# Kernel optimization log

Measured on AMD Instinct MI355X. Metric: run time of the kernel, lower is better.

## Reference

```python
import jax, jax.numpy as jnp
import numpy as np

K = 15  # window_size


def setup_inputs() -> dict:
    key = jax.random.key(0)
    k1, k2, k3, k4 = jax.random.split(key, 4)
    x = jax.random.normal(k1, (8, 256, 240, 240), dtype=jnp.float32)
    wq = jax.random.normal(k2, (144, 256), dtype=jnp.float32) * (1.0 / np.sqrt(256))
    wk = jax.random.normal(k3, (144, 256), dtype=jnp.float32) * (1.0 / np.sqrt(256))
    wproj = jax.random.normal(k4, (256, 256), dtype=jnp.float32) * (1.0 / np.sqrt(256))
    return {"x": x, "wq": wq, "wk": wk, "wproj": wproj}


def _pnlm(x, wq, wk, wproj):
    b, c, h, w = x.shape
    ph, pw = (-h) % K, (-w) % K
    if ph or pw:
        x_pad = jnp.pad(x, ((0, 0), (0, 0), (0, ph), (0, pw)), mode='reflect')
    else:
        x_pad = x
    H, W = x_pad.shape[2], x_pad.shape[3]
    nh, nw = H // K, W // K
    N = K * K  # tokens per window
    # blockify: (B,C,H,W) -> (B*nh*nw, C, N)
    blocks = (x_pad.reshape(b, c, nh, K, nw, K)
              .transpose(0, 2, 4, 1, 3, 5)
              .reshape(b * nh * nw, c, N))
    q = jnp.einsum('ec,bcn->bne', wq, blocks)   # (B', N, E)
    km = jnp.einsum('ec,bcm->bem', wk, blocks)  # (B', E, N)
    att = jnp.einsum('bne,bem->bnm', q, km)     # (B', N, N)
    scale = 1.0 / jnp.sqrt(jnp.asarray(q.shape[-1], dtype=att.dtype))
    att = jax.nn.softmax(att * scale, axis=-1)
    y = jnp.einsum('bnm,bcm->bcn', att, blocks)  # att @ V, V = blocks^T
    y = jnp.einsum('oc,bcn->bon', wproj, y)      # 1x1 proj_out
    # unblockify: (B', C, N) -> (B, C, H, W)
    y = (y.reshape(b, nh, nw, c, K, K)
         .transpose(0, 3, 1, 4, 2, 5)
         .reshape(b, c, H, W))
    y = y[:, :, :h, :w]
    return x + y


def reference(x, wq, wk, wproj):
    return _pnlm(x, wq, wk, wproj)
```

## Files before the change

kernel.cpp:

```cpp
#include <hip/hip_runtime.h>


typedef __bf16 bf16x8 __attribute__((ext_vector_type(8)));
typedef float  f32x4  __attribute__((ext_vector_type(4)));

#define MFMA(a,b,c) __builtin_amdgcn_mfma_f32_16x16x32_bf16((a),(b),(c),0,0,0)

#define QK_ROW 320
#define KL_STRIDE 168
#define XBB_ROW 240

__device__ __forceinline__ unsigned short f2bf(float f){
  union { float f; unsigned int u; } v; v.f = f;
  unsigned int r = v.u + 0x7FFFu + ((v.u >> 16) & 1u);
  return (unsigned short)(r >> 16);
}
__device__ __forceinline__ float bf2f(unsigned short u){
  union { unsigned int u; float f; } v; v.u = ((unsigned int)u) << 16;
  return v.f;
}
__device__ __forceinline__ int swz(int row, int col){
  return row*256 + ((((col >> 3) ^ (row & 7)) << 3) | (col & 7));
}
__device__ __forceinline__ int swzC(int row, int col){
  return row*256 + (col ^ ((((row >> 3) ^ row) & 7) << 3));
}
__device__ __forceinline__ bf16x8 ld_frag_lds(const unsigned short* p, int idx){
  uint4 v = *(const uint4*)(p + idx);
  return __builtin_bit_cast(bf16x8, v);
}
__device__ __forceinline__ bf16x8 ld_frag_b(const void* p){
  uint4 v = *(const uint4*)(p);
  return __builtin_bit_cast(bf16x8, v);
}

__device__ __forceinline__ void repack_frag(const unsigned int* plo, const unsigned int* phi,
                                            uint4* outf, int lane){
  const int nn = lane & 15, hh = lane >> 4;
  const int sla = nn + 32*(hh & 1);
  const int slb = sla + 16;
  const bool up = hh >= 2;
  #pragma unroll
  for (int k = 0; k < 8; ++k){
    unsigned int a0 = (unsigned int)__shfl((int)plo[2*k],   sla);
    unsigned int a1 = (unsigned int)__shfl((int)plo[2*k+1], sla);
    unsigned int b0 = (unsigned int)__shfl((int)phi[2*k],   sla);
    unsigned int b1 = (unsigned int)__shfl((int)phi[2*k+1], sla);
    unsigned int c0 = (unsigned int)__shfl((int)plo[2*k],   slb);
    unsigned int c1 = (unsigned int)__shfl((int)plo[2*k+1], slb);
    unsigned int d0 = (unsigned int)__shfl((int)phi[2*k],   slb);
    unsigned int d1 = (unsigned int)__shfl((int)phi[2*k+1], slb);
    outf[k] = make_uint4(up?a1:a0, up?b1:b0, up?c1:c0, up?d1:d0);
  }
}

__global__ __launch_bounds__(256) void k_w(
    const float* __restrict__ wq, const float* __restrict__ wk,
    const float* __restrict__ wproj,
    unsigned short* __restrict__ wqb, unsigned short* __restrict__ wkb,
    unsigned short* __restrict__ wpb)
{
  int i = blockIdx.x*256 + threadIdx.x;
  if (i < 20480){
    int e = i >> 7, c = (i & 127)*2;
    unsigned int v = 0;
    if (e < 144) v = (unsigned int)f2bf(wq[e*256+c]) | ((unsigned int)f2bf(wq[e*256+c+1]) << 16);
    *(unsigned int*)(wqb + (size_t)i*2) = v;
  } else if (i < 40960){
    int j = i - 20480;
    int e = j >> 7, c = (j & 127)*2;
    unsigned int v = 0;
    if (e < 144) v = (unsigned int)f2bf(wk[e*256+c]) | ((unsigned int)f2bf(wk[e*256+c+1]) << 16);
    *(unsigned int*)(wkb + (size_t)j*2) = v;
  } else if (i < 73728){
    int l = i - 40960;
    int o = l >> 7, c = (l & 127)*2;
    *(unsigned int*)(wpb + (size_t)l*2) =
        (unsigned int)f2bf(wproj[o*256+c]) | ((unsigned int)f2bf(wproj[o*256+c+1]) << 16);
  }
}

__global__ __launch_bounds__(256) void k_xb(
    const float* __restrict__ x, unsigned short* __restrict__ xbb)
{
  __shared__ unsigned short xs[8*15*240];
  const int wg = blockIdx.x;
  const int cg = wg & 31;
  const int th = (wg >> 5) & 15;
  const int b  = wg >> 9;
  const int tid = threadIdx.x;

  const float* xb = x + ((size_t)b*256 + cg*8)*57600 + th*15*240;
  for (int i = tid; i < 8*15*120; i += 256){
    int c = i / 1800;
    int rem = i - c*1800;
    int r = rem / 120, p2 = rem - r*120;
    float2 v = *(const float2*)(xb + (size_t)c*57600 + r*240 + p2*2);
    *(unsigned int*)(&xs[(c*15 + r)*240 + p2*2]) =
        (unsigned int)f2bf(v.x) | ((unsigned int)f2bf(v.y) << 16);
  }
  __syncthreads();

  for (int i = tid; i < 8*16*30; i += 256){
    int c = i / 480;
    int rem = i - c*480;
    int tw = rem / 30, ch = rem - tw*30;
    union { unsigned short u16[8]; uint4 u4; } pk;
    #pragma unroll
    for (int j = 0; j < 8; ++j){
      int m = ch*8 + j;
      int r = m / 15, s = m - r*15;
      pk.u16[j] = (m <= 224) ? xs[(c*15 + r)*240 + tw*15 + s] : (unsigned short)0;
    }
    *(uint4*)(xbb + ((size_t)(b*256 + th*16 + tw)*256 + cg*8 + c)*XBB_ROW + ch*8) = pk.u4;
  }
}

__global__ __launch_bounds__(512) void k_qkb(
    const unsigned short* __restrict__ xbb,
    const unsigned short* __restrict__ wqb, const unsigned short* __restrict__ wkb,
    unsigned short* __restrict__ qkws)
{
  __shared__ __align__(16) unsigned short S[32768];
  unsigned short* xt  = S;
  unsigned short* wqs = S;
  unsigned short* wks = S + 8192;
  const int wg = blockIdx.x;
  const int b  = wg >> 8;
  const int th = (wg >> 4) & 15, tw = wg & 15;
  const int h0 = th*15, w0 = tw*15;
  const int tid = threadIdx.x;
  const int lane = tid & 63, wave = tid >> 6;
  const int col  = lane & 15, hi = lane >> 4;
  const unsigned short* xbw = xbb + (size_t)wg * (256*XBB_ROW);

  #pragma unroll 1
  for (int half = 0; half < 2; ++half){
    if (half) __syncthreads();
    for (int i = tid; i < 256*16; i += 512){
      int c = i >> 4, m8 = i & 15;
      int m = half*128 + m8*8;
      if (m < 240){
        uint4 v = *(const uint4*)(xbw + (size_t)c*XBB_ROW + m);
        const unsigned short* pv = (const unsigned short*)&v;
        #pragma unroll
        for (int j = 0; j < 8; ++j)
          xt[swzC(m8*8 + j, c)] = pv[j];
      }
    }
    __syncthreads();

    const int t = half*8 + wave;
    const bool act = t < 15;
    bf16x8 af[8];
    if (act){
      const int rloc = wave*16 + col;
      #pragma unroll
      for (int k = 0; k < 8; ++k)
        af[k] = ld_frag_lds(xt, swzC(rloc, k*32 + hi*8));
    }
    __syncthreads();

    #pragma unroll 1
    for (int eg = 0; eg < 5; ++eg){
      if (eg) __syncthreads();
      for (int i = tid; i < 32*32; i += 512){
        int e_l = i >> 5, c8 = (i & 31)*8;
        size_t off = (size_t)(eg*32 + e_l)*256 + c8;
        *(uint4*)(&wqs[swz(e_l, c8)]) = *(const uint4*)(wqb + off);
        *(uint4*)(&wks[swz(e_l, c8)]) = *(const uint4*)(wkb + off);
      }
      __syncthreads();
      if (act){
        #pragma unroll
        for (int et = 0; et < 2; ++et){
          f32x4 aq = {0.f,0.f,0.f,0.f}, ak = {0.f,0.f,0.f,0.f};
          const int el = et*16 + col;
          #pragma unroll
          for (int k = 0; k < 8; ++k){
            int idx = swz(el, k*32 + hi*8);
            bf16x8 bq = ld_frag_lds(wqs, idx);
            bf16x8 bk = ld_frag_lds(wks, idx);
            aq = MFMA(af[k], bq, aq);
            ak = MFMA(af[k], bk, ak);
          }
          const int e_out = eg*32 + et*16 + col;
          #pragma unroll
          for (int jj = 0; jj < 4; ++jj){
            int m_px = t*16 + hi*4 + jj;
            if (m_px <= 224){
              int hw = (h0 + m_px/15)*240 + w0 + m_px%15;
              size_t row = ((size_t)b*57600 + hw)*QK_ROW;
              qkws[row + e_out]       = f2bf(aq[jj]);
              qkws[row + 160 + e_out] = f2bf(ak[jj]);
            }
          }
        }
      }
    }
  }
}

__global__ __launch_bounds__(512) void k_qk(
    const float* __restrict__ x, const float* __restrict__ wq,
    const float* __restrict__ wk,
    unsigned short* __restrict__ qkws)
{
  __shared__ __align__(16) unsigned short S[32768];
  unsigned short* xt  = S;
  unsigned short* wqs = S;
  unsigned short* wks = S + 8192;
  const int wg  = blockIdx.x;
  const int b   = wg / 450;
  const int hw0 = (wg % 450) * 128;
  const int tid = threadIdx.x;
  const int lane = tid & 63, wave = tid >> 6;
  const int col  = lane & 15, hi = lane >> 4;

  {
    const float* xb = x + (size_t)b * 256 * 57600 + hw0;
    const int hw_l = tid & 127;
    #pragma unroll 4
    for (int i = 0; i < 32; ++i){
      int c = ((tid >> 7) * 32 + i) * 2;
      float f0 = xb[(size_t)c     * 57600 + hw_l];
      float f1 = xb[(size_t)(c+1) * 57600 + hw_l];
      *(unsigned int*)(&xt[swz(hw_l, c)]) =
          (unsigned int)f2bf(f0) | ((unsigned int)f2bf(f1) << 16);
    }
  }
  __syncthreads();

  bf16x8 af[8];
  const int arow = wave*16 + col;
  #pragma unroll
  for (int k = 0; k < 8; ++k)
    af[k] = ld_frag_lds(xt, swz(arow, k*32 + hi*8));

  const size_t orow_base = (size_t)b*57600 + hw0 + wave*16;

  for (int eg = 0; eg < 5; ++eg){
    __syncthreads();
    for (int i = 0; i < 8; ++i){
      int idx = tid + i*512;
      int e_l = idx >> 7, c = (idx & 127) * 2;
      int e = eg*32 + e_l;
      float2 vq = make_float2(0.f,0.f), vk = make_float2(0.f,0.f);
      if (e < 144){
        vq = *(const float2*)(wq + (size_t)e*256 + c);
        vk = *(const float2*)(wk + (size_t)e*256 + c);
      }
      *(unsigned int*)(&wqs[swz(e_l, c)]) =
          (unsigned int)f2bf(vq.x) | ((unsigned int)f2bf(vq.y) << 16);
      *(unsigned int*)(&wks[swz(e_l, c)]) =
          (unsigned int)f2bf(vk.x) | ((unsigned int)f2bf(vk.y) << 16);
    }
    __syncthreads();
    #pragma unroll
    for (int etl = 0; etl < 2; ++etl){
      f32x4 aq = {0.f,0.f,0.f,0.f}, ak = {0.f,0.f,0.f,0.f};
      const int el = etl*16 + col;
      #pragma unroll
      for (int k = 0; k < 8; ++k){
        int idx = swz(el, k*32 + hi*8);
        bf16x8 bq = ld_frag_lds(wqs, idx);
        bf16x8 bk = ld_frag_lds(wks, idx);
        aq = MFMA(af[k], bq, aq);
        ak = MFMA(af[k], bk, ak);
      }
      const int e_out = eg*32 + etl*16 + col;
      #pragma unroll
      for (int jj = 0; jj < 4; ++jj){
        size_t row = orow_base + hi*4 + jj;
        qkws[row*QK_ROW + e_out]       = f2bf(aq[jj]);
        qkws[row*QK_ROW + 160 + e_out] = f2bf(ak[jj]);
      }
    }
  }
}

__global__ __launch_bounds__(512,4) void k_attn_b(
    const unsigned short* __restrict__ xbb, const float* __restrict__ wproj,
    const unsigned short* __restrict__ qkws, float* __restrict__ out)
{
  __shared__ __align__(16) unsigned short S[40320 + 480];
  unsigned short* kl = S;
  unsigned short* xl = S;
  unsigned short* wl = S + 32768;
  unsigned int*  hwp = (unsigned int*)(S + 40320);
  const int wg = blockIdx.x;
  const int b  = wg >> 8;
  const int th = (wg >> 4) & 15, tw = wg & 15;
  const int h0 = th*15, w0 = tw*15;
  const int tid = threadIdx.x;
  const int lane = tid & 63, wave = tid >> 6;
  const int col  = lane & 15, hi = lane >> 4;
  const size_t obase = (size_t)b * 256 * 57600;
  const unsigned short* qkb = qkws + (size_t)b * 57600 * QK_ROW;
  const unsigned short* xbw = xbb + (size_t)wg * (256*XBB_ROW);

  if (tid < 240){
    int ms = tid <= 224 ? tid : 224;
    hwp[tid] = (unsigned int)((h0 + ms/15)*240 + w0 + ms%15);
  }
  __syncthreads();

  for (int i = tid; i < 240*20; i += 512){
    int m = i / 20, eb = i - m*20;
    *(uint4*)(&kl[m*KL_STRIDE + eb*8]) =
        *(const uint4*)(qkb + (size_t)hwp[m]*QK_ROW + 160 + eb*8);
  }
  __syncthreads();

  uint4 attf[2][8];
  #pragma unroll
  for (int slot = 0; slot < 2; ++slot){
    const int nt = wave + slot*8;
    if (nt < 15){
      const int n  = nt*16 + col;
      const int na = n <= 224 ? n : 224;
      const unsigned short* qrow = qkb + (size_t)hwp[na]*QK_ROW;
      bf16x8 qf[5];
      #pragma unroll
      for (int c = 0; c < 5; ++c)
        qf[c] = ld_frag_b(qrow + c*32 + hi*8);
      f32x4 at[15];
      #pragma unroll
      for (int T = 0; T < 15; ++T){
        f32x4 acc = {0.f,0.f,0.f,0.f};
        #pragma unroll
        for (int c = 0; c < 5; ++c){
          bf16x8 kf = ld_frag_lds(kl, (T*16 + col)*KL_STRIDE + c*32 + hi*8);
          acc = MFMA(kf, qf[c], acc);
        }
        at[T] = acc;
      }
      const float sc = 0.12022458674074695f;
      float M = -3.0e38f;
      #pragma unroll
      for (int T = 0; T < 15; ++T){
        #pragma unroll
        for (int jj = 0; jj < 4; ++jj){
          int m = T*16 + hi*4 + jj;
          if (m <= 224) M = fmaxf(M, at[T][jj]*sc);
        }
      }
      M = fmaxf(M, __shfl_xor(M, 16));
      M = fmaxf(M, __shfl_xor(M, 32));
      float Ssum = 0.f;
      #pragma unroll
      for (int T = 0; T < 15; ++T){
        #pragma unroll
        for (int jj = 0; jj < 4; ++jj){
          int m = T*16 + hi*4 + jj;
          float v = (m <= 224) ? exp2f(at[T][jj]*sc - M) : 0.f;
          at[T][jj] = v; Ssum += v;
        }
      }
      Ssum += __shfl_xor(Ssum, 16);
      Ssum += __shfl_xor(Ssum, 32);
      const float inv = 1.0f / Ssum;
      unsigned int plo[16], phi[16];
      #pragma unroll
      for (int T = 0; T < 15; ++T){
        plo[T] = (unsigned int)f2bf(at[T][0]*inv) | ((unsigned int)f2bf(at[T][1]*inv) << 16);
        phi[T] = (unsigned int)f2bf(at[T][2]*inv) | ((unsigned int)f2bf(at[T][3]*inv) << 16);
      }
      plo[15] = 0u; phi[15] = 0u;
      repack_frag(plo, phi, attf[slot], lane);
    }
  }

  unsigned int ylo[2][16], yhi[2][16];
  #pragma unroll
  for (int half = 0; half < 2; ++half){
    __syncthreads();
    for (int i = tid; i < 128*32; i += 512){
      int c = i >> 5, m8 = i & 31;
      uint4 v = make_uint4(0u,0u,0u,0u);
      if (m8 < 30)
        v = *(const uint4*)(xbw + (size_t)(half*128 + c)*XBB_ROW + m8*8);
      *(uint4*)(&xl[swz(c, m8*8)]) = v;
    }
    __syncthreads();
    #pragma unroll
    for (int slot = 0; slot < 2; ++slot){
      const int nt = wave + slot*8;
      if (nt < 15){
        #pragma unroll
        for (int ct = 0; ct < 8; ++ct){
          f32x4 acc = {0.f,0.f,0.f,0.f};
          #pragma unroll
          for (int k = 0; k < 8; ++k){
            bf16x8 xf = ld_frag_lds(xl, swz(ct*16 + col, k*32 + hi*8));
            acc = MFMA(xf, __builtin_bit_cast(bf16x8, attf[slot][k]), acc);
          }
          ylo[slot][half*8 + ct] = (unsigned int)f2bf(acc[0]) | ((unsigned int)f2bf(acc[1]) << 16);
          yhi[slot][half*8 + ct] = (unsigned int)f2bf(acc[2]) | ((unsigned int)f2bf(acc[3]) << 16);
        }
      }
    }
  }

  uint4 y1f[2][8];
  #pragma unroll
  for (int slot = 0; slot < 2; ++slot){
    const int nt = wave + slot*8;
    if (nt < 15)
      repack_frag(ylo[slot], yhi[slot], y1f[slot], lane);
  }

  #pragma unroll 1
  for (int oe = 0; oe < 16; ++oe){
    __syncthreads();
    for (int i = tid; i < 16*128; i += 512){
      int olr = i >> 7, c = (i & 127)*2;
      const float* wr = wproj + (size_t)(oe*16 + olr)*256 + c;
      *(unsigned int*)(&wl[swz(olr, c)]) =
          (unsigned int)f2bf(wr[0]) | ((unsigned int)f2bf(wr[1]) << 16);
    }
    __syncthreads();
    bf16x8 awf[8];
    #pragma unroll
    for (int k = 0; k < 8; ++k)
      awf[k] = ld_frag_lds(wl, swz(col, k*32 + hi*8));
    #pragma unroll
    for (int slot = 0; slot < 2; ++slot){
      const int nt = wave + slot*8;
      if (nt < 15){
        f32x4 y2 = {0.f,0.f,0.f,0.f};
        #pragma unroll
        for (int k = 0; k < 8; ++k)
          y2 = MFMA(awf[k], __builtin_bit_cast(bf16x8, y1f[slot][k]), y2);
        const int n = nt*16 + col;
        if (n <= 224){
          const size_t pix = hwp[n];
          #pragma unroll
          for (int jj = 0; jj < 4; ++jj){
            int o = oe*16 + hi*4 + jj;
            float xr = bf2f(xbw[(size_t)o*XBB_ROW + n]);
            out[obase + (size_t)o*57600 + pix] = y2[jj] + xr;
          }
        }
      }
    }
  }
}

__global__ __launch_bounds__(512,4) void k_attn_s(
    const float* __restrict__ x, const float* __restrict__ wproj,
    const unsigned short* __restrict__ qkws, float* __restrict__ out)
{
  __shared__ __align__(16) unsigned short S[40320 + 480];
  unsigned short* kl = S;
  unsigned short* xl = S;
  unsigned short* wl = S + 32768;
  unsigned int*  hwp = (unsigned int*)(S + 40320);
  const int wg = blockIdx.x;
  const int b  = wg >> 8;
  const int th = (wg >> 4) & 15, tw = wg & 15;
  const int h0 = th*15, w0 = tw*15;
  const int tid = threadIdx.x;
  const int lane = tid & 63, wave = tid >> 6;
  const int col  = lane & 15, hi = lane >> 4;
  const size_t xbase = (size_t)b * 256 * 57600;
  const unsigned short* qkb = qkws + (size_t)b * 57600 * QK_ROW;

  if (tid < 240){
    int ms = tid <= 224 ? tid : 224;
    hwp[tid] = (unsigned int)((h0 + ms/15)*240 + w0 + ms%15);
  }
  __syncthreads();

  for (int i = tid; i < 240*20; i += 512){
    int m = i / 20, eb = i - m*20;
    *(uint4*)(&kl[m*KL_STRIDE + eb*8]) =
        *(const uint4*)(qkb + (size_t)hwp[m]*QK_ROW + 160 + eb*8);
  }
  __syncthreads();

  uint4 attf[2][8];
  #pragma unroll
  for (int slot = 0; slot < 2; ++slot){
    const int nt = wave + slot*8;
    if (nt < 15){
      const int n  = nt*16 + col;
      const int na = n <= 224 ? n : 224;
      const unsigned short* qrow = qkb + (size_t)hwp[na]*QK_ROW;
      bf16x8 qf[5];
      #pragma unroll
      for (int c = 0; c < 5; ++c)
        qf[c] = ld_frag_b(qrow + c*32 + hi*8);
      f32x4 at[15];
      #pragma unroll
      for (int T = 0; T < 15; ++T){
        f32x4 acc = {0.f,0.f,0.f,0.f};
        #pragma unroll
        for (int c = 0; c < 5; ++c){
          bf16x8 kf = ld_frag_lds(kl, (T*16 + col)*KL_STRIDE + c*32 + hi*8);
          acc = MFMA(kf, qf[c], acc);
        }
        at[T] = acc;
      }
      const float sc = 0.12022458674074695f;
      float M = -3.0e38f;
      #pragma unroll
      for (int T = 0; T < 15; ++T){
        #pragma unroll
        for (int jj = 0; jj < 4; ++jj){
          int m = T*16 + hi*4 + jj;
          if (m <= 224) M = fmaxf(M, at[T][jj]*sc);
        }
      }
      M = fmaxf(M, __shfl_xor(M, 16));
      M = fmaxf(M, __shfl_xor(M, 32));
      float Ssum = 0.f;
      #pragma unroll
      for (int T = 0; T < 15; ++T){
        #pragma unroll
        for (int jj = 0; jj < 4; ++jj){
          int m = T*16 + hi*4 + jj;
          float v = (m <= 224) ? exp2f(at[T][jj]*sc - M) : 0.f;
          at[T][jj] = v; Ssum += v;
        }
      }
      Ssum += __shfl_xor(Ssum, 16);
      Ssum += __shfl_xor(Ssum, 32);
      const float inv = 1.0f / Ssum;
      unsigned int plo[16], phi[16];
      #pragma unroll
      for (int T = 0; T < 15; ++T){
        plo[T] = (unsigned int)f2bf(at[T][0]*inv) | ((unsigned int)f2bf(at[T][1]*inv) << 16);
        phi[T] = (unsigned int)f2bf(at[T][2]*inv) | ((unsigned int)f2bf(at[T][3]*inv) << 16);
      }
      plo[15] = 0u; phi[15] = 0u;
      repack_frag(plo, phi, attf[slot], lane);
    }
  }

  unsigned int ylo[2][16], yhi[2][16];
  #pragma unroll
  for (int half = 0; half < 2; ++half){
    __syncthreads();
    for (int i = tid; i < 128*128; i += 512){
      int c = i >> 7, m = (i & 127)*2;
      int m0 = m <= 224 ? m : 224;
      float f0 = (m     <= 224) ? x[xbase + (size_t)(half*128 + c)*57600 + hwp[m0]]   : 0.f;
      float f1 = (m + 1 <= 224) ? x[xbase + (size_t)(half*128 + c)*57600 + hwp[m0+1]] : 0.f;
      *(unsigned int*)(&xl[swz(c, m)]) =
          (unsigned int)f2bf(f0) | ((unsigned int)f2bf(f1) << 16);
    }
    __syncthreads();
    #pragma unroll
    for (int slot = 0; slot < 2; ++slot){
      const int nt = wave + slot*8;
      if (nt < 15){
        #pragma unroll
        for (int ct = 0; ct < 8; ++ct){
          f32x4 acc = {0.f,0.f,0.f,0.f};
          #pragma unroll
          for (int k = 0; k < 8; ++k){
            bf16x8 xf = ld_frag_lds(xl, swz(ct*16 + col, k*32 + hi*8));
            acc = MFMA(xf, __builtin_bit_cast(bf16x8, attf[slot][k]), acc);
          }
          ylo[slot][half*8 + ct] = (unsigned int)f2bf(acc[0]) | ((unsigned int)f2bf(acc[1]) << 16);
          yhi[slot][half*8 + ct] = (unsigned int)f2bf(acc[2]) | ((unsigned int)f2bf(acc[3]) << 16);
        }
      }
    }
  }

  uint4 y1f[2][8];
  #pragma unroll
  for (int slot = 0; slot < 2; ++slot){
    const int nt = wave + slot*8;
    if (nt < 15)
      repack_frag(ylo[slot], yhi[slot], y1f[slot], lane);
  }

  #pragma unroll 1
  for (int oe = 0; oe < 16; ++oe){
    __syncthreads();
    for (int i = tid; i < 16*128; i += 512){
      int olr = i >> 7, c = (i & 127)*2;
      const float* wr = wproj + (size_t)(oe*16 + olr)*256 + c;
      *(unsigned int*)(&wl[swz(olr, c)]) =
          (unsigned int)f2bf(wr[0]) | ((unsigned int)f2bf(wr[1]) << 16);
    }
    __syncthreads();
    bf16x8 awf[8];
    #pragma unroll
    for (int k = 0; k < 8; ++k)
      awf[k] = ld_frag_lds(wl, swz(col, k*32 + hi*8));
    #pragma unroll
    for (int slot = 0; slot < 2; ++slot){
      const int nt = wave + slot*8;
      if (nt < 15){
        f32x4 y2 = {0.f,0.f,0.f,0.f};
        #pragma unroll
        for (int k = 0; k < 8; ++k)
          y2 = MFMA(awf[k], __builtin_bit_cast(bf16x8, y1f[slot][k]), y2);
        const int n = nt*16 + col;
        if (n <= 224){
          const size_t pix = hwp[n];
          #pragma unroll
          for (int jj = 0; jj < 4; ++jj){
            int o = oe*16 + hi*4 + jj;
            const size_t idx = xbase + (size_t)o*57600 + pix;
            out[idx] = y2[jj] + x[idx];
          }
        }
      }
    }
  }
}

extern "C" void kernel_launch(void* const* d_in, const int* in_sizes, int n_in,
                              void* d_out, int out_size, void* d_ws, size_t ws_size,
                              hipStream_t stream)
{
  const float* x     = (const float*)d_in[0];
  const float* wq    = (const float*)d_in[1];
  const float* wk    = (const float*)d_in[2];
  const float* wproj = (const float*)d_in[3];
  float* out = (float*)d_out;
  (void)in_sizes; (void)n_in; (void)out_size;

  const size_t QKWS_B = (size_t)8*57600*QK_ROW*2;
  const size_t XBB_B  = (size_t)8*256*256*XBB_ROW*2;
  const size_t WQB_B  = (size_t)160*256*2;
  const size_t WKB_B  = (size_t)160*256*2;
  const size_t WPB_B  = (size_t)256*256*2;
  unsigned short* qkws = (unsigned short*)d_ws;

  if (ws_size >= QKWS_B + XBB_B + WQB_B + WKB_B + WPB_B){
    unsigned short* xbb = (unsigned short*)((char*)d_ws + QKWS_B);
    unsigned short* wqb = (unsigned short*)((char*)d_ws + QKWS_B + XBB_B);
    unsigned short* wkb = wqb + 160*256;
    unsigned short* wpb = wkb + 160*256;
    k_w     <<<dim3(288),  dim3(256), 0, stream>>>(wq, wk, wproj, wqb, wkb, wpb);
    k_xb    <<<dim3(4096), dim3(256), 0, stream>>>(x, xbb);
    k_qkb   <<<dim3(2048), dim3(512), 0, stream>>>(xbb, wqb, wkb, qkws);
    k_attn_b<<<dim3(2048), dim3(512), 0, stream>>>(xbb, wproj, qkws, out);
  } else if (ws_size >= QKWS_B + XBB_B){
    unsigned short* xbb = (unsigned short*)((char*)d_ws + QKWS_B);
    k_xb    <<<dim3(4096), dim3(256), 0, stream>>>(x, xbb);
    k_qk    <<<dim3(3600), dim3(512), 0, stream>>>(x, wq, wk, qkws);
    k_attn_b<<<dim3(2048), dim3(512), 0, stream>>>(xbb, wproj, qkws, out);
  } else {
    k_qk    <<<dim3(3600), dim3(512), 0, stream>>>(x, wq, wk, qkws);
    k_attn_s<<<dim3(2048), dim3(512), 0, stream>>>(x, wproj, qkws, out);
  }
}
```

Before: 1.040 ms.

## Reuse weight tiles across both pixel halves and use pre-converted bf16 proj weights

In k_qkb, the x fragments for both pixel halves are now held in registers, so each wq/wk tile is staged to LDS once per block instead of twice. k_attn_b now reads the pre-converted bf16 wproj with 16-byte loads instead of converting fp32 weights per block. It also processes 32 output channels per staging step, which halves the proj-loop barriers, and it hoists the pixel indices. The risks are higher register pressure from the doubled af fragments and the extra pixs/awf state, which could lower occupancy.

```diff
diff --git a/kernel.cpp b/kernel.cpp
--- a/kernel.cpp
+++ b/kernel.cpp
@@ -134,13 +134,14 @@
   const int col  = lane & 15, hi = lane >> 4;
   const unsigned short* xbw = xbb + (size_t)wg * (256*XBB_ROW);
 
+  bf16x8 af[2][8];
   #pragma unroll 1
   for (int half = 0; half < 2; ++half){
     if (half) __syncthreads();
     for (int i = tid; i < 256*16; i += 512){
       int c = i >> 4, m8 = i & 15;
       int m = half*128 + m8*8;
-      if (m < 240){
+      if (m + 8 <= 240){
         uint4 v = *(const uint4*)(xbw + (size_t)c*XBB_ROW + m);
         const unsigned short* pv = (const unsigned short*)&v;
         #pragma unroll
@@ -149,29 +150,33 @@
       }
     }
     __syncthreads();
-
-    const int t = half*8 + wave;
-    const bool act = t < 15;
-    bf16x8 af[8];
-    if (act){
-      const int rloc = wave*16 + col;
+    const int rloc = wave*16 + col;
+    if (half == 0){
       #pragma unroll
       for (int k = 0; k < 8; ++k)
-        af[k] = ld_frag_lds(xt, swzC(rloc, k*32 + hi*8));
-    }
-    __syncthreads();
-
-    #pragma unroll 1
-    for (int eg = 0; eg < 5; ++eg){
-      if (eg) __syncthreads();
-      for (int i = tid; i < 32*32; i += 512){
-        int e_l = i >> 5, c8 = (i & 31)*8;
-        size_t off = (size_t)(eg*32 + e_l)*256 + c8;
-        *(uint4*)(&wqs[swz(e_l, c8)]) = *(const uint4*)(wqb + off);
-        *(uint4*)(&wks[swz(e_l, c8)]) = *(const uint4*)(wkb + off);
-      }
-      __syncthreads();
-      if (act){
+        af[0][k] = ld_frag_lds(xt, swzC(rloc, k*32 + hi*8));
+    } else {
+      #pragma unroll
+      for (int k = 0; k < 8; ++k)
+        af[1][k] = ld_frag_lds(xt, swzC(rloc, k*32 + hi*8));
+    }
+  }
+  __syncthreads();
+
+  #pragma unroll 1
+  for (int eg = 0; eg < 5; ++eg){
+    if (eg) __syncthreads();
+    for (int i = tid; i < 32*32; i += 512){
+      int e_l = i >> 5, c8 = (i & 31)*8;
+      size_t off = (size_t)(eg*32 + e_l)*256 + c8;
+      *(uint4*)(&wqs[swz(e_l, c8)]) = *(const uint4*)(wqb + off);
+      *(uint4*)(&wks[swz(e_l, c8)]) = *(const uint4*)(wkb + off);
+    }
+    __syncthreads();
+    #pragma unroll
+    for (int h2 = 0; h2 < 2; ++h2){
+      const int t = h2*8 + wave;
+      if (t < 15){
         #pragma unroll
         for (int et = 0; et < 2; ++et){
           f32x4 aq = {0.f,0.f,0.f,0.f}, ak = {0.f,0.f,0.f,0.f};
@@ -181,8 +186,8 @@
             int idx = swz(el, k*32 + hi*8);
             bf16x8 bq = ld_frag_lds(wqs, idx);
             bf16x8 bk = ld_frag_lds(wks, idx);
-            aq = MFMA(af[k], bq, aq);
-            ak = MFMA(af[k], bk, ak);
+            aq = MFMA(af[h2][k], bq, aq);
+            ak = MFMA(af[h2][k], bk, ak);
           }
           const int e_out = eg*32 + et*16 + col;
           #pragma unroll
@@ -193,6 +198,184 @@
               size_t row = ((size_t)b*57600 + hw)*QK_ROW;
               qkws[row + e_out]       = f2bf(aq[jj]);
               qkws[row + 160 + e_out] = f2bf(ak[jj]);
+            }
+          }
+        }
+      }
+    }
+  }
+}
+
+__global__ __launch_bounds__(512,4) void k_attn_b(
+    const unsigned short* __restrict__ xbb, const unsigned short* __restrict__ wpb,
+    const unsigned short* __restrict__ qkws, float* __restrict__ out)
+{
+  __shared__ __align__(16) unsigned short S[40960];
+  unsigned short* kl = S;
+  unsigned short* xl = S;
+  unsigned short* wl = S + 32768;
+  unsigned int*  hwp = (unsigned int*)(S + 40320);
+  const int wg = blockIdx.x;
+  const int b  = wg >> 8;
+  const int th = (wg >> 4) & 15, tw = wg & 15;
+  const int h0 = th*15, w0 = tw*15;
+  const int tid = threadIdx.x;
+  const int lane = tid & 63, wave = tid >> 6;
+  const int col  = lane & 15, hi = lane >> 4;
+  const size_t obase = (size_t)b * 256 * 57600;
+  const unsigned short* qkb = qkws + (size_t)b * 57600 * QK_ROW;
+  const unsigned short* xbw = xbb + (size_t)wg * (256*XBB_ROW);
+
+  if (tid < 240){
+    int ms = tid <= 224 ? tid : 224;
+    hwp[tid] = (unsigned int)((h0 + ms/15)*240 + w0 + ms%15);
+  }
+  __syncthreads();
+
+  for (int i = tid; i < 240*20; i += 512){
+    int m = i / 20, eb = i - m*20;
+    *(uint4*)(&kl[m*KL_STRIDE + eb*8]) =
+        *(const uint4*)(qkb + (size_t)hwp[m]*QK_ROW + 160 + eb*8);
+  }
+  __syncthreads();
+
+  uint4 attf[2][8];
+  #pragma unroll
+  for (int slot = 0; slot < 2; ++slot){
+    const int nt = wave + slot*8;
+    if (nt < 15){
+      const int n  = nt*16 + col;
+      const int na = n <= 224 ? n : 224;
+      const unsigned short* qrow = qkb + (size_t)hwp[na]*QK_ROW;
+      bf16x8 qf[5];
+      #pragma unroll
+      for (int c = 0; c < 5; ++c)
+        qf[c] = ld_frag_b(qrow + c*32 + hi*8);
+      f32x4 at[15];
+      #pragma unroll
+      for (int T = 0; T < 15; ++T){
+        f32x4 acc = {0.f,0.f,0.f,0.f};
+        #pragma unroll
+        for (int c = 0; c < 5; ++c){
+          bf16x8 kf = ld_frag_lds(kl, (T*16 + col)*KL_STRIDE + c*32 + hi*8);
+          acc = MFMA(kf, qf[c], acc);
+        }
+        at[T] = acc;
+      }
+      const float sc = 0.12022458674074695f;
+      float M = -3.0e38f;
+      #pragma unroll
+      for (int T = 0; T < 15; ++T){
+        #pragma unroll
+        for (int jj = 0; jj < 4; ++jj){
+          int m = T*16 + hi*4 + jj;
+          if (m <= 224) M = fmaxf(M, at[T][jj]*sc);
+        }
+      }
+      M = fmaxf(M, __shfl_xor(M, 16));
+      M = fmaxf(M, __shfl_xor(M, 32));
+      float Ssum = 0.f;
+      #pragma unroll
+      for (int T = 0; T < 15; ++T){
+        #pragma unroll
+        for (int jj = 0; jj < 4; ++jj){
+          int m = T*16 + hi*4 + jj;
+          float v = (m <= 224) ? exp2f(at[T][jj]*sc - M) : 0.f;
+          at[T][jj] = v; Ssum += v;
+        }
+      }
+      Ssum += __shfl_xor(Ssum, 16);
+      Ssum += __shfl_xor(Ssum, 32);
+      const float inv = 1.0f / Ssum;
+      unsigned int plo[16], phi[16];
+      #pragma unroll
+      for (int T = 0; T < 15; ++T){
+        plo[T] = (unsigned int)f2bf(at[T][0]*inv) | ((unsigned int)f2bf(at[T][1]*inv) << 16);
+        phi[T] = (unsigned int)f2bf(at[T][2]*inv) | ((unsigned int)f2bf(at[T][3]*inv) << 16);
+      }
+      plo[15] = 0u; phi[15] = 0u;
+      repack_frag(plo, phi, attf[slot], lane);
+    }
+  }
+
+  int pixs[2];
+  #pragma unroll
+  for (int slot = 0; slot < 2; ++slot){
+    const int n = (wave + slot*8)*16 + col;
+    pixs[slot] = (n <= 224) ? (int)hwp[n] : -1;
+  }
+
+  unsigned int ylo[2][16], yhi[2][16];
+  #pragma unroll
+  for (int half = 0; half < 2; ++half){
+    __syncthreads();
+    for (int i = tid; i < 128*32; i += 512){
+      int c = i >> 5, m8 = i & 31;
+      uint4 v = make_uint4(0u,0u,0u,0u);
+      if (m8 < 30)
+        v = *(const uint4*)(xbw + (size_t)(half*128 + c)*XBB_ROW + m8*8);
+      *(uint4*)(&xl[swz(c, m8*8)]) = v;
+    }
+    __syncthreads();
+    #pragma unroll
+    for (int slot = 0; slot < 2; ++slot){
+      const int nt = wave + slot*8;
+      if (nt < 15){
+        #pragma unroll
+        for (int ct = 0; ct < 8; ++ct){
+          f32x4 acc = {0.f,0.f,0.f,0.f};
+          #pragma unroll
+          for (int k = 0; k < 8; ++k){
+            bf16x8 xf = ld_frag_lds(xl, swz(ct*16 + col, k*32 + hi*8));
+            acc = MFMA(xf, __builtin_bit_cast(bf16x8, attf[slot][k]), acc);
+          }
+          ylo[slot][half*8 + ct] = (unsigned int)f2bf(acc[0]) | ((unsigned int)f2bf(acc[1]) << 16);
+          yhi[slot][half*8 + ct] = (unsigned int)f2bf(acc[2]) | ((unsigned int)f2bf(acc[3]) << 16);
+        }
+      }
+    }
+  }
+
+  uint4 y1f[2][8];
+  #pragma unroll
+  for (int slot = 0; slot < 2; ++slot){
+    const int nt = wave + slot*8;
+    if (nt < 15)
+      repack_frag(ylo[slot], yhi[slot], y1f[slot], lane);
+  }
+
+  #pragma unroll 1
+  for (int oe = 0; oe < 8; ++oe){
+    __syncthreads();
+    for (int i = tid; i < 32*32; i += 512){
+      int olr = i >> 5, c8 = (i & 31)*8;
+      *(uint4*)(&wl[swz(olr, c8)]) =
+          *(const uint4*)(wpb + (size_t)(oe*32 + olr)*256 + c8);
+    }
+    __syncthreads();
+    #pragma unroll
+    for (int ot = 0; ot < 2; ++ot){
+      bf16x8 awf[8];
+      const int olr = ot*16 + col;
+      #pragma unroll
+      for (int k = 0; k < 8; ++k)
+        awf[k] = ld_frag_lds(wl, swz(olr, k*32 + hi*8));
+      #pragma unroll
+      for (int slot = 0; slot < 2; ++slot){
+        const int nt = wave + slot*8;
+        if (nt < 15){
+          f32x4 y2 = {0.f,0.f,0.f,0.f};
+          #pragma unroll
+          for (int k = 0; k < 8; ++k)
+            y2 = MFMA(awf[k], __builtin_bit_cast(bf16x8, y1f[slot][k]), y2);
+          const int n = nt*16 + col;
+          if (n <= 224){
+            const size_t pix = (size_t)pixs[slot];
+            #pragma unroll
+            for (int jj = 0; jj < 4; ++jj){
+              int o = oe*32 + ot*16 + hi*4 + jj;
+              float xr = bf2f(xbw[(size_t)o*XBB_ROW + n]);
+              out[obase + (size_t)o*57600 + pix] = y2[jj] + xr;
             }
           }
         }
@@ -274,174 +457,6 @@
         size_t row = orow_base + hi*4 + jj;
         qkws[row*QK_ROW + e_out]       = f2bf(aq[jj]);
         qkws[row*QK_ROW + 160 + e_out] = f2bf(ak[jj]);
-      }
-    }
-  }
-}
-
-__global__ __launch_bounds__(512,4) void k_attn_b(
-    const unsigned short* __restrict__ xbb, const float* __restrict__ wproj,
-    const unsigned short* __restrict__ qkws, float* __restrict__ out)
-{
-  __shared__ __align__(16) unsigned short S[40320 + 480];
-  unsigned short* kl = S;
-  unsigned short* xl = S;
-  unsigned short* wl = S + 32768;
-  unsigned int*  hwp = (unsigned int*)(S + 40320);
-  const int wg = blockIdx.x;
-  const int b  = wg >> 8;
-  const int th = (wg >> 4) & 15, tw = wg & 15;
-  const int h0 = th*15, w0 = tw*15;
-  const int tid = threadIdx.x;
-  const int lane = tid & 63, wave = tid >> 6;
-  const int col  = lane & 15, hi = lane >> 4;
-  const size_t obase = (size_t)b * 256 * 57600;
-  const unsigned short* qkb = qkws + (size_t)b * 57600 * QK_ROW;
-  const unsigned short* xbw = xbb + (size_t)wg * (256*XBB_ROW);
-
-  if (tid < 240){
-    int ms = tid <= 224 ? tid : 224;
-    hwp[tid] = (unsigned int)((h0 + ms/15)*240 + w0 + ms%15);
-  }
-  __syncthreads();
-
-  for (int i = tid; i < 240*20; i += 512){
-    int m = i / 20, eb = i - m*20;
-    *(uint4*)(&kl[m*KL_STRIDE + eb*8]) =
-        *(const uint4*)(qkb + (size_t)hwp[m]*QK_ROW + 160 + eb*8);
-  }
-  __syncthreads();
-
-  uint4 attf[2][8];
-  #pragma unroll
-  for (int slot = 0; slot < 2; ++slot){
-    const int nt = wave + slot*8;
-    if (nt < 15){
-      const int n  = nt*16 + col;
-      const int na = n <= 224 ? n : 224;
-      const unsigned short* qrow = qkb + (size_t)hwp[na]*QK_ROW;
-      bf16x8 qf[5];
-      #pragma unroll
-      for (int c = 0; c < 5; ++c)
-        qf[c] = ld_frag_b(qrow + c*32 + hi*8);
-      f32x4 at[15];
-      #pragma unroll
-      for (int T = 0; T < 15; ++T){
-        f32x4 acc = {0.f,0.f,0.f,0.f};
-        #pragma unroll
-        for (int c = 0; c < 5; ++c){
-          bf16x8 kf = ld_frag_lds(kl, (T*16 + col)*KL_STRIDE + c*32 + hi*8);
-          acc = MFMA(kf, qf[c], acc);
-        }
-        at[T] = acc;
-      }
-      const float sc = 0.12022458674074695f;
-      float M = -3.0e38f;
-      #pragma unroll
-      for (int T = 0; T < 15; ++T){
-        #pragma unroll
-        for (int jj = 0; jj < 4; ++jj){
-          int m = T*16 + hi*4 + jj;
-          if (m <= 224) M = fmaxf(M, at[T][jj]*sc);
-        }
-      }
-      M = fmaxf(M, __shfl_xor(M, 16));
-      M = fmaxf(M, __shfl_xor(M, 32));
-      float Ssum = 0.f;
-      #pragma unroll
-      for (int T = 0; T < 15; ++T){
-        #pragma unroll
-        for (int jj = 0; jj < 4; ++jj){
-          int m = T*16 + hi*4 + jj;
-          float v = (m <= 224) ? exp2f(at[T][jj]*sc - M) : 0.f;
-          at[T][jj] = v; Ssum += v;
-        }
-      }
-      Ssum += __shfl_xor(Ssum, 16);
-      Ssum += __shfl_xor(Ssum, 32);
-      const float inv = 1.0f / Ssum;
-      unsigned int plo[16], phi[16];
-      #pragma unroll
-      for (int T = 0; T < 15; ++T){
-        plo[T] = (unsigned int)f2bf(at[T][0]*inv) | ((unsigned int)f2bf(at[T][1]*inv) << 16);
-        phi[T] = (unsigned int)f2bf(at[T][2]*inv) | ((unsigned int)f2bf(at[T][3]*inv) << 16);
-      }
-      plo[15] = 0u; phi[15] = 0u;
-      repack_frag(plo, phi, attf[slot], lane);
-    }
-  }
-
-  unsigned int ylo[2][16], yhi[2][16];
-  #pragma unroll
-  for (int half = 0; half < 2; ++half){
-    __syncthreads();
-    for (int i = tid; i < 128*32; i += 512){
-      int c = i >> 5, m8 = i & 31;
-      uint4 v = make_uint4(0u,0u,0u,0u);
-      if (m8 < 30)
-        v = *(const uint4*)(xbw + (size_t)(half*128 + c)*XBB_ROW + m8*8);
-      *(uint4*)(&xl[swz(c, m8*8)]) = v;
-    }
-    __syncthreads();
-    #pragma unroll
-    for (int slot = 0; slot < 2; ++slot){
-      const int nt = wave + slot*8;
-      if (nt < 15){
-        #pragma unroll
-        for (int ct = 0; ct < 8; ++ct){
-          f32x4 acc = {0.f,0.f,0.f,0.f};
-          #pragma unroll
-          for (int k = 0; k < 8; ++k){
-            bf16x8 xf = ld_frag_lds(xl, swz(ct*16 + col, k*32 + hi*8));
-            acc = MFMA(xf, __builtin_bit_cast(bf16x8, attf[slot][k]), acc);
-          }
-          ylo[slot][half*8 + ct] = (unsigned int)f2bf(acc[0]) | ((unsigned int)f2bf(acc[1]) << 16);
-          yhi[slot][half*8 + ct] = (unsigned int)f2bf(acc[2]) | ((unsigned int)f2bf(acc[3]) << 16);
-        }
-      }
-    }
-  }
-
-  uint4 y1f[2][8];
-  #pragma unroll
-  for (int slot = 0; slot < 2; ++slot){
-    const int nt = wave + slot*8;
-    if (nt < 15)
-      repack_frag(ylo[slot], yhi[slot], y1f[slot], lane);
-  }
-
-  #pragma unroll 1
-  for (int oe = 0; oe < 16; ++oe){
-    __syncthreads();
-    for (int i = tid; i < 16*128; i += 512){
-      int olr = i >> 7, c = (i & 127)*2;
-      const float* wr = wproj + (size_t)(oe*16 + olr)*256 + c;
-      *(unsigned int*)(&wl[swz(olr, c)]) =
-          (unsigned int)f2bf(wr[0]) | ((unsigned int)f2bf(wr[1]) << 16);
-    }
-    __syncthreads();
-    bf16x8 awf[8];
-    #pragma unroll
-    for (int k = 0; k < 8; ++k)
-      awf[k] = ld_frag_lds(wl, swz(col, k*32 + hi*8));
-    #pragma unroll
-    for (int slot = 0; slot < 2; ++slot){
-      const int nt = wave + slot*8;
-      if (nt < 15){
-        f32x4 y2 = {0.f,0.f,0.f,0.f};
-        #pragma unroll
-        for (int k = 0; k < 8; ++k)
-          y2 = MFMA(awf[k], __builtin_bit_cast(bf16x8, y1f[slot][k]), y2);
-        const int n = nt*16 + col;
-        if (n <= 224){
-          const size_t pix = hwp[n];
-          #pragma unroll
-          for (int jj = 0; jj < 4; ++jj){
-            int o = oe*16 + hi*4 + jj;
-            float xr = bf2f(xbw[(size_t)o*XBB_ROW + n]);
-            out[obase + (size_t)o*57600 + pix] = y2[jj] + xr;
-          }
-        }
       }
     }
   }
@@ -628,12 +643,10 @@
 
   const size_t QKWS_B = (size_t)8*57600*QK_ROW*2;
   const size_t XBB_B  = (size_t)8*256*256*XBB_ROW*2;
-  const size_t WQB_B  = (size_t)160*256*2;
-  const size_t WKB_B  = (size_t)160*256*2;
-  const size_t WPB_B  = (size_t)256*256*2;
+  const size_t WB_ALL = (size_t)(160*256 + 160*256 + 256*256)*2;
   unsigned short* qkws = (unsigned short*)d_ws;
 
-  if (ws_size >= QKWS_B + XBB_B + WQB_B + WKB_B + WPB_B){
+  if (ws_size >= QKWS_B + XBB_B + WB_ALL){
     unsigned short* xbb = (unsigned short*)((char*)d_ws + QKWS_B);
     unsigned short* wqb = (unsigned short*)((char*)d_ws + QKWS_B + XBB_B);
     unsigned short* wkb = wqb + 160*256;
@@ -641,12 +654,7 @@
     k_w     <<<dim3(288),  dim3(256), 0, stream>>>(wq, wk, wproj, wqb, wkb, wpb);
     k_xb    <<<dim3(4096), dim3(256), 0, stream>>>(x, xbb);
     k_qkb   <<<dim3(2048), dim3(512), 0, stream>>>(xbb, wqb, wkb, qkws);
-    k_attn_b<<<dim3(2048), dim3(512), 0, stream>>>(xbb, wproj, qkws, out);
-  } else if (ws_size >= QKWS_B + XBB_B){
-    unsigned short* xbb = (unsigned short*)((char*)d_ws + QKWS_B);
-    k_xb    <<<dim3(4096), dim3(256), 0, stream>>>(x, xbb);
-    k_qk    <<<dim3(3600), dim3(512), 0, stream>>>(x, wq, wk, qkws);
-    k_attn_b<<<dim3(2048), dim3(512), 0, stream>>>(xbb, wproj, qkws, out);
+    k_attn_b<<<dim3(2048), dim3(512), 0, stream>>>(xbb, wpb, qkws, out);
   } else {
     k_qk    <<<dim3(3600), dim3(512), 0, stream>>>(x, wq, wk, qkws);
     k_attn_s<<<dim3(2048), dim3(512), 0, stream>>>(x, wproj, qkws, out);
```

After: 954.5 us. 8.2% less time.
